# Kernel optimization log

Measured on AMD Instinct MI355X. Metric: run time of the kernel, lower is better.

The kernel has to match this reference:

```python
import jax, jax.numpy as jnp
import numpy as np

B, N, D, R = 4, 2048, 1024, 64
LN_EPS = 1e-5


def setup_inputs() -> dict:
    key = jax.random.key(0)
    k_x, k_m, k_u, k_v = jax.random.split(key, 4)
    x = jax.random.normal(k_x, (B, N, D), dtype=jnp.float32)
    mask = jax.random.uniform(k_m, (B, N, R), dtype=jnp.float32)
    # xavier-style init for low-rank bases U_max, V_max: (d_model, R_max)
    scale = jnp.sqrt(2.0 / (D + R)).astype(jnp.float32)
    U = jax.random.normal(k_u, (D, R), dtype=jnp.float32) * scale
    V = jax.random.normal(k_v, (D, R), dtype=jnp.float32) * scale
    gamma = jnp.ones((D,), dtype=jnp.float32)
    beta = jnp.zeros((D,), dtype=jnp.float32)
    return {"x": x, "mask": mask, "U": U, "V": V, "gamma": gamma, "beta": beta}


def _layernorm(y, gamma, beta):
    mu = jnp.mean(y, axis=-1, keepdims=True)
    var = jnp.mean(jnp.square(y - mu), axis=-1, keepdims=True)
    return (y - mu) * jax.lax.rsqrt(var + LN_EPS) * gamma + beta


def reference(x, mask, U, V, gamma, beta):
    # Q/K: low-rank projections gated by per-token continuous mask
    Q = jnp.einsum('bnd,dr->bnr', x, U) * mask            # (B, N, R)
    K = jnp.einsum('bnd,dr->bnr', x, V) * mask            # (B, N, R)
    # effective rank per query token, clamped at 1
    r_eff = jnp.maximum(jnp.sum(mask, axis=-1, keepdims=True), 1.0)  # (B, N, 1)
    scores = jnp.einsum('bqr,bkr->bqk', Q, K) / jnp.sqrt(r_eff)      # (B, N, N)
    A = jax.nn.softmax(scores, axis=-1)
    delta = jnp.einsum('bqk,bkd->bqd', A, x)              # (B, N, D)
    # backbone is identity: out = LN(x + delta)
    return _layernorm(x + delta, gamma, beta)
```

## Files before the change

kernel.cpp:

```cpp
#include <hip/hip_runtime.h>

#define Bb 4
#define Nn 2048
#define Dd 1024
#define Rr 64
#define LN_EPS 1e-5f

typedef unsigned short u16;
typedef short bf16x8 __attribute__((ext_vector_type(8)));
typedef float f32x4 __attribute__((ext_vector_type(4)));

__device__ __forceinline__ u16 f2bf(float f) {
  unsigned u = __float_as_uint(f);
  u += 0x7FFFu + ((u >> 16) & 1u);
  return (u16)(u >> 16);
}

__device__ __forceinline__ void g2l16(u16* l, const u16* g) {
  __builtin_amdgcn_global_load_lds(
      (const __attribute__((address_space(1))) unsigned int*)g,
      (__attribute__((address_space(3))) unsigned int*)l, 16, 0, 0);
}

__global__ __launch_bounds__(256) void prep_fused(const float* __restrict__ x,
    u16* __restrict__ xt, u16* __restrict__ xb, const float* __restrict__ U,
    const float* __restrict__ V, const float* __restrict__ mask,
    u16* __restrict__ uvt, float* __restrict__ qs) {
  __shared__ float tile[64][65];
  const int bid = blockIdx.x;
  const int t = threadIdx.x;
  if (bid < 2048) {
    const int b = bid >> 9;
    const int d0 = ((bid >> 5) & 15) * 64;
    const int n0 = (bid & 31) * 64;
    const int c = t & 63, r4 = t >> 6;
#pragma unroll
    for (int rr = 0; rr < 16; rr++) {
      int row = rr * 4 + r4;
      tile[row][c] = x[(size_t)(b * Nn + n0 + row) * Dd + d0 + c];
    }
    __syncthreads();
    const int c2 = t & 31, r8 = t >> 5;
#pragma unroll
    for (int rr = 0; rr < 8; rr++) {
      int dd = rr * 8 + r8;
      unsigned lo = f2bf(tile[2 * c2][dd]);
      unsigned hi = f2bf(tile[2 * c2 + 1][dd]);
      *(unsigned*)&xt[(size_t)(b * Dd + d0 + dd) * Nn + n0 + 2 * c2] = lo | (hi << 16);
    }
#pragma unroll
    for (int rr = 0; rr < 8; rr++) {
      int row = rr * 8 + r8;
      unsigned lo = f2bf(tile[row][2 * c2]);
      unsigned hi = f2bf(tile[row][2 * c2 + 1]);
      *(unsigned*)&xb[(size_t)(b * Nn + n0 + row) * Dd + d0 + 2 * c2] = lo | (hi << 16);
    }
  } else if (bid < 2080) {
    const int sub = bid - 2048;
    const int which = sub >> 4;
    const int d0 = (sub & 15) * 64;
    const float* src = which ? V : U;
    const int c = t & 63, r4 = t >> 6;
#pragma unroll
    for (int rr = 0; rr < 16; rr++) {
      int row = rr * 4 + r4;
      tile[row][c] = src[(size_t)(d0 + row) * Rr + c];
    }
    __syncthreads();
#pragma unroll
    for (int rr = 0; rr < 16; rr++) {
      int r = rr * 4 + r4;
      uvt[(size_t)(which * 64 + r) * Dd + d0 + c] = f2bf(tile[c][r]);
    }
  } else {
    const int row = (bid - 2080) * 4 + (t >> 6);
    const int lane = t & 63;
    float v = mask[(size_t)row * Rr + lane];
#pragma unroll
    for (int off = 32; off; off >>= 1) v += __shfl_xor(v, off);
    if (lane == 0) qs[row] = rsqrtf(fmaxf(v, 1.0f));
  }
}

__global__ __launch_bounds__(256) void proj_qk(const u16* __restrict__ xb,
    const float* __restrict__ mask, const u16* __restrict__ uvt,
    u16* __restrict__ Qo, u16* __restrict__ Ko) {
  const int t = threadIdx.x;
  const int w = t >> 6, l = t & 63, quad = l >> 4, l16 = l & 15;
  const int g0 = blockIdx.x * 32;
  f32x4 acc[2][2];
#pragma unroll
  for (int i = 0; i < 2; i++)
#pragma unroll
    for (int j = 0; j < 2; j++) acc[i][j] = (f32x4){0.f, 0.f, 0.f, 0.f};
  for (int k0 = 0; k0 < Dd; k0 += 32) {
    bf16x8 a[2];
#pragma unroll
    for (int mt = 0; mt < 2; mt++)
      a[mt] = *(const bf16x8*)&xb[(size_t)(g0 + mt * 16 + l16) * Dd + k0 + quad * 8];
    bf16x8 bfr[2];
#pragma unroll
    for (int i = 0; i < 2; i++) {
      int col = (w * 2 + i) * 16 + l16;
      bfr[i] = *(const bf16x8*)&uvt[(size_t)col * Dd + k0 + quad * 8];
    }
#pragma unroll
    for (int mt = 0; mt < 2; mt++)
#pragma unroll
      for (int i = 0; i < 2; i++)
        acc[mt][i] = __builtin_amdgcn_mfma_f32_16x16x32_bf16(a[mt], bfr[i], acc[mt][i], 0, 0, 0);
  }
#pragma unroll
  for (int mt = 0; mt < 2; mt++)
#pragma unroll
    for (int i = 0; i < 2; i++) {
      int col = (w * 2 + i) * 16 + l16;
      int r_ = col & 63;
#pragma unroll
      for (int r = 0; r < 4; r++) {
        int row = g0 + mt * 16 + quad * 4 + r;
        float v = acc[mt][i][r] * mask[(size_t)row * Rr + r_];
        u16 bv = f2bf(v);
        if (col < 64) Qo[(size_t)row * Rr + r_] = bv;
        else          Ko[(size_t)row * Rr + r_] = bv;
      }
    }
}

__global__ __launch_bounds__(512, 2) void score_softmax(
    const u16* __restrict__ Qm, const u16* __restrict__ Km,
    const float* __restrict__ qs, u16* __restrict__ Pw,
    float* __restrict__ linv_g) {
  __shared__ float red[32][8];
  __shared__ float mfin[32];
  __shared__ __align__(16) u16 Ps[8][32][264];
  const int t = threadIdx.x;
  const int w = t >> 6, l = t & 63, quad = l >> 4, l16 = l & 15;
  const int id = blockIdx.x;
  const int xcd = id & 7;
  const int b = xcd >> 1;
  const int q0 = (((id >> 3) << 1) | (xcd & 1)) * 32;
  bf16x8 qf[2][2];
#pragma unroll
  for (int mt = 0; mt < 2; mt++)
#pragma unroll
    for (int ks = 0; ks < 2; ks++)
      qf[mt][ks] = *(const bf16x8*)&Qm[(size_t)(b * Nn + q0 + mt * 16 + l16) * Rr + ks * 32 + quad * 8];
  f32x4 acc[2][16];
#pragma unroll
  for (int mt = 0; mt < 2; mt++)
#pragma unroll
    for (int nt = 0; nt < 16; nt++) acc[mt][nt] = (f32x4){0.f, 0.f, 0.f, 0.f};
#pragma unroll
  for (int nt = 0; nt < 16; nt++) {
#pragma unroll
    for (int ks = 0; ks < 2; ks++) {
      bf16x8 kf = *(const bf16x8*)&Km[(size_t)(b * Nn + w * 256 + nt * 16 + l16) * Rr + ks * 32 + quad * 8];
#pragma unroll
      for (int mt = 0; mt < 2; mt++)
        acc[mt][nt] = __builtin_amdgcn_mfma_f32_16x16x32_bf16(qf[mt][ks], kf, acc[mt][nt], 0, 0, 0);
    }
  }
  float sc[2][4];
#pragma unroll
  for (int mt = 0; mt < 2; mt++)
#pragma unroll
    for (int r = 0; r < 4; r++)
      sc[mt][r] = qs[(size_t)b * Nn + q0 + mt * 16 + quad * 4 + r];
#pragma unroll
  for (int mt = 0; mt < 2; mt++)
#pragma unroll
    for (int nt = 0; nt < 16; nt++)
#pragma unroll
      for (int r = 0; r < 4; r++) acc[mt][nt][r] *= sc[mt][r];
  float vmax[2][4];
#pragma unroll
  for (int mt = 0; mt < 2; mt++)
#pragma unroll
    for (int r = 0; r < 4; r++) {
      float m = -1e30f;
#pragma unroll
      for (int nt = 0; nt < 16; nt++) m = fmaxf(m, acc[mt][nt][r]);
#pragma unroll
      for (int off = 1; off < 16; off <<= 1) m = fmaxf(m, __shfl_xor(m, off));
      vmax[mt][r] = m;
    }
  if (l16 == 0) {
#pragma unroll
    for (int mt = 0; mt < 2; mt++)
#pragma unroll
      for (int r = 0; r < 4; r++) red[mt * 16 + quad * 4 + r][w] = vmax[mt][r];
  }
  __syncthreads();
  if (t < 32) {
    float m = -1e30f;
#pragma unroll
    for (int i = 0; i < 8; i++) m = fmaxf(m, red[t][i]);
    mfin[t] = m;
  }
  __syncthreads();
  float rowm[2][4], vsum[2][4];
#pragma unroll
  for (int mt = 0; mt < 2; mt++)
#pragma unroll
    for (int r = 0; r < 4; r++) {
      rowm[mt][r] = mfin[mt * 16 + quad * 4 + r];
      vsum[mt][r] = 0.f;
    }
#pragma unroll
  for (int mt = 0; mt < 2; mt++)
#pragma unroll
    for (int nt = 0; nt < 16; nt++)
#pragma unroll
      for (int r = 0; r < 4; r++) {
        float p = __expf(acc[mt][nt][r] - rowm[mt][r]);
        acc[mt][nt][r] = p;
        vsum[mt][r] += p;
      }
#pragma unroll
  for (int mt = 0; mt < 2; mt++)
#pragma unroll
    for (int r = 0; r < 4; r++) {
#pragma unroll
      for (int off = 1; off < 16; off <<= 1) vsum[mt][r] += __shfl_xor(vsum[mt][r], off);
    }
  __syncthreads();
  if (l16 == 0) {
#pragma unroll
    for (int mt = 0; mt < 2; mt++)
#pragma unroll
      for (int r = 0; r < 4; r++) red[mt * 16 + quad * 4 + r][w] = vsum[mt][r];
  }
  __syncthreads();
  if (t < 32) {
    float s = 0.f;
#pragma unroll
    for (int i = 0; i < 8; i++) s += red[t][i];
    linv_g[(size_t)b * Nn + q0 + t] = 1.f / s;
  }
#pragma unroll
  for (int mt = 0; mt < 2; mt++)
#pragma unroll
    for (int nt = 0; nt < 16; nt++)
#pragma unroll
      for (int r = 0; r < 4; r++)
        Ps[w][mt * 16 + quad * 4 + r][nt * 16 + l16] = f2bf(acc[mt][nt][r]);
  const int rrow = l >> 3, rcol = (l & 7) * 8;
#pragma unroll
  for (int rr = 0; rr < 4; rr++)
#pragma unroll
    for (int cc = 0; cc < 4; cc++) {
      const int row = rr * 8 + rrow;
      const int col = cc * 64 + rcol;
      bf16x8 v = *(const bf16x8*)&Ps[w][row][col];
      *(bf16x8*)&Pw[(size_t)(b * Nn + q0 + row) * Nn + w * 256 + col] = v;
    }
}

__global__ __launch_bounds__(512, 4) void pv_gemm(
    const u16* __restrict__ Pw, const u16* __restrict__ xt,
    const float* __restrict__ x, const float* __restrict__ linv_g,
    float* __restrict__ y) {
  __shared__ u16 As[2][128 * 64];
  __shared__ u16 Bs[2][128 * 64];
  const int t = threadIdx.x;
  const int w = t >> 6, l = t & 63, quad = l >> 4, l16 = l & 15;
  const int id = blockIdx.x;
  const int xcd = id & 7;
  const int b = xcd >> 1;
  const int nh = xcd & 1;
  const int rest = id >> 3;
  const int m0 = (rest & 15) * 128;
  const int n0 = (nh * 4 + (rest >> 4)) * 128;
  const int lrow = l >> 3;
  const int srow = w * 8 + lrow;
  const int skoff = ((l & 7) ^ lrow) * 8;
  const size_t gA = (size_t)(b * Nn + m0 + srow) * Nn + skoff;
  const size_t gB = (size_t)(b * Dd + n0 + srow) * Nn + skoff;
  const int wm = w >> 2, wn = w & 3;
  const int sw = l16 & 7;
  f32x4 acc[4][2];
#pragma unroll
  for (int i = 0; i < 4; i++)
#pragma unroll
    for (int j = 0; j < 2; j++) acc[i][j] = (f32x4){0.f, 0.f, 0.f, 0.f};

#define STAGE(bf, k0)                                              \
  do {                                                             \
    g2l16(&As[bf][(w * 8) * 64],      &Pw[gA + (size_t)(k0)]);     \
    g2l16(&As[bf][(64 + w * 8) * 64], &Pw[gA + 64 * Nn + (size_t)(k0)]); \
    g2l16(&Bs[bf][(w * 8) * 64],      &xt[gB + (size_t)(k0)]);     \
    g2l16(&Bs[bf][(64 + w * 8) * 64], &xt[gB + 64 * Nn + (size_t)(k0)]); \
  } while (0)

  STAGE(0, 0);
  for (int kt = 0; kt < Nn / 64; kt++) {
    const int cur = kt & 1;
    if (kt + 1 < Nn / 64) {
      STAGE(cur ^ 1, (kt + 1) * 64);
      asm volatile("s_waitcnt vmcnt(4)" ::: "memory");
    } else {
      asm volatile("s_waitcnt vmcnt(0)" ::: "memory");
    }
    __builtin_amdgcn_s_barrier();
    asm volatile("" ::: "memory");
#pragma unroll
    for (int ks = 0; ks < 2; ks++) {
      const int slot = ((ks * 4 + quad) ^ sw) * 8;
      bf16x8 af[4], bf_[2];
#pragma unroll
      for (int mt = 0; mt < 4; mt++)
        af[mt] = *(const bf16x8*)&As[cur][(wm * 64 + mt * 16 + l16) * 64 + slot];
#pragma unroll
      for (int nt = 0; nt < 2; nt++)
        bf_[nt] = *(const bf16x8*)&Bs[cur][(wn * 32 + nt * 16 + l16) * 64 + slot];
#pragma unroll
      for (int mt = 0; mt < 4; mt++)
#pragma unroll
        for (int nt = 0; nt < 2; nt++)
          acc[mt][nt] = __builtin_amdgcn_mfma_f32_16x16x32_bf16(af[mt], bf_[nt], acc[mt][nt], 0, 0, 0);
    }
    asm volatile("" ::: "memory");
    __builtin_amdgcn_s_barrier();
  }
#undef STAGE
  float li[4][4];
#pragma unroll
  for (int mt = 0; mt < 4; mt++)
#pragma unroll
    for (int r = 0; r < 4; r++)
      li[mt][r] = linv_g[(size_t)b * Nn + m0 + wm * 64 + mt * 16 + quad * 4 + r];
#pragma unroll
  for (int mt = 0; mt < 4; mt++)
#pragma unroll
    for (int nt = 0; nt < 2; nt++) {
      const int nn = n0 + wn * 32 + nt * 16 + l16;
#pragma unroll
      for (int r = 0; r < 4; r++) {
        const int m = m0 + wm * 64 + mt * 16 + quad * 4 + r;
        const size_t off = ((size_t)(b * Nn + m)) * Dd + nn;
        y[off] = x[off] + li[mt][r] * acc[mt][nt][r];
      }
    }
}

__global__ __launch_bounds__(256) void ln_k(float* __restrict__ y,
    const float* __restrict__ gamma, const float* __restrict__ beta) {
  const int row = blockIdx.x * 4 + (threadIdx.x >> 6);
  const int l = threadIdx.x & 63;
  float* p = y + (size_t)row * Dd;
  float4 v[4];
  float s = 0.f, q = 0.f;
#pragma unroll
  for (int i = 0; i < 4; i++) {
    v[i] = ((const float4*)p)[i * 64 + l];
    s += v[i].x + v[i].y + v[i].z + v[i].w;
    q += v[i].x * v[i].x + v[i].y * v[i].y + v[i].z * v[i].z + v[i].w * v[i].w;
  }
#pragma unroll
  for (int off = 32; off; off >>= 1) {
    s += __shfl_xor(s, off);
    q += __shfl_xor(q, off);
  }
  float mu = s * (1.f / Dd);
  float var = q * (1.f / Dd) - mu * mu;
  float rstd = rsqrtf(var + LN_EPS);
#pragma unroll
  for (int i = 0; i < 4; i++) {
    float4 g = ((const float4*)gamma)[i * 64 + l];
    float4 be = ((const float4*)beta)[i * 64 + l];
    v[i].x = (v[i].x - mu) * rstd * g.x + be.x;
    v[i].y = (v[i].y - mu) * rstd * g.y + be.y;
    v[i].z = (v[i].z - mu) * rstd * g.z + be.z;
    v[i].w = (v[i].w - mu) * rstd * g.w + be.w;
    ((float4*)p)[i * 64 + l] = v[i];
  }
}

extern "C" void kernel_launch(void* const* d_in, const int* in_sizes, int n_in,
                              void* d_out, int out_size, void* d_ws, size_t ws_size,
                              hipStream_t stream) {
  const float* x     = (const float*)d_in[0];
  const float* mask  = (const float*)d_in[1];
  const float* U     = (const float*)d_in[2];
  const float* V     = (const float*)d_in[3];
  const float* gamma = (const float*)d_in[4];
  const float* beta  = (const float*)d_in[5];
  float* out = (float*)d_out;
  char* ws = (char*)d_ws;
  u16*   xt   = (u16*)ws;
  u16*   Qw   = (u16*)(ws + (size_t)(16 << 20));
  u16*   Kw   = (u16*)(ws + (size_t)(17 << 20));
  u16*   uvt  = (u16*)(ws + (size_t)(18 << 20));
  float* qsb  = (float*)(ws + (size_t)(18 << 20) + (256 << 10));
  float* linv = (float*)(ws + (size_t)(18 << 20) + (288 << 10));
  u16*   Pw   = (u16*)(ws + (size_t)(19 << 20));
  u16*   xb   = Pw;

  prep_fused   <<<4128, 256, 0, stream>>>(x, xt, xb, U, V, mask, uvt, qsb);
  proj_qk      <<<(Bb * Nn) / 32, 256, 0, stream>>>(xb, mask, uvt, Qw, Kw);
  score_softmax<<<Bb * (Nn / 32), 512, 0, stream>>>(Qw, Kw, qsb, Pw, linv);
  pv_gemm      <<<Bb * (Nn / 128) * (Dd / 128), 512, 0, stream>>>(Pw, xt, x, linv, out);
  ln_k         <<<Bb * Nn / 4, 256, 0, stream>>>(out, gamma, beta);
}
```

Before: 185.7 us.

## Recompute QK scores inside PV GEMM instead of materializing probability matrix

The score kernel now computes only the row max and inverse sum and no longer writes the bf16 probability matrix P (B×N×N). The PV kernel recomputes QK^T per 64-key tile with MFMA, applies exp with the stored max, scale and 1/sum, stages P through per-wave LDS, and multiplies it by x. This removes a large write and read of P to and from HBM. In exchange, each n-tile block repeats the score computation (D/128 = 8 times per query row), and the per-warp tiling changes from 4x2 to 1x8 MFMA tiles.

```diff
diff --git a/kernel.cpp b/kernel.cpp
--- a/kernel.cpp
+++ b/kernel.cpp
@@ -127,13 +127,12 @@
     }
 }
 
-__global__ __launch_bounds__(512, 2) void score_softmax(
+__global__ __launch_bounds__(512, 2) void score_ml(
     const u16* __restrict__ Qm, const u16* __restrict__ Km,
-    const float* __restrict__ qs, u16* __restrict__ Pw,
+    const float* __restrict__ qs, float* __restrict__ mx_g,
     float* __restrict__ linv_g) {
-  __shared__ float red[32][8];
-  __shared__ float mfin[32];
-  __shared__ __align__(16) u16 Ps[8][32][264];
+  __shared__ __align__(16) float red[32][8];
+  __shared__ __align__(16) float mfin[32];
   const int t = threadIdx.x;
   const int w = t >> 6, l = t & 63, quad = l >> 4, l16 = l & 15;
   const int id = blockIdx.x;
@@ -197,6 +196,7 @@
 #pragma unroll
     for (int i = 0; i < 8; i++) m = fmaxf(m, red[t][i]);
     mfin[t] = m;
+    mx_g[(size_t)b * Nn + q0 + t] = m;
   }
   __syncthreads();
   float rowm[2][4], vsum[2][4];
@@ -212,11 +212,8 @@
 #pragma unroll
     for (int nt = 0; nt < 16; nt++)
 #pragma unroll
-      for (int r = 0; r < 4; r++) {
-        float p = __expf(acc[mt][nt][r] - rowm[mt][r]);
-        acc[mt][nt][r] = p;
-        vsum[mt][r] += p;
-      }
+      for (int r = 0; r < 4; r++)
+        vsum[mt][r] += __expf(acc[mt][nt][r] - rowm[mt][r]);
 #pragma unroll
   for (int mt = 0; mt < 2; mt++)
 #pragma unroll
@@ -238,31 +235,16 @@
     for (int i = 0; i < 8; i++) s += red[t][i];
     linv_g[(size_t)b * Nn + q0 + t] = 1.f / s;
   }
-#pragma unroll
-  for (int mt = 0; mt < 2; mt++)
-#pragma unroll
-    for (int nt = 0; nt < 16; nt++)
-#pragma unroll
-      for (int r = 0; r < 4; r++)
-        Ps[w][mt * 16 + quad * 4 + r][nt * 16 + l16] = f2bf(acc[mt][nt][r]);
-  const int rrow = l >> 3, rcol = (l & 7) * 8;
-#pragma unroll
-  for (int rr = 0; rr < 4; rr++)
-#pragma unroll
-    for (int cc = 0; cc < 4; cc++) {
-      const int row = rr * 8 + rrow;
-      const int col = cc * 64 + rcol;
-      bf16x8 v = *(const bf16x8*)&Ps[w][row][col];
-      *(bf16x8*)&Pw[(size_t)(b * Nn + q0 + row) * Nn + w * 256 + col] = v;
-    }
-}
-
-__global__ __launch_bounds__(512, 4) void pv_gemm(
-    const u16* __restrict__ Pw, const u16* __restrict__ xt,
-    const float* __restrict__ x, const float* __restrict__ linv_g,
-    float* __restrict__ y) {
-  __shared__ u16 As[2][128 * 64];
-  __shared__ u16 Bs[2][128 * 64];
+}
+
+__global__ __launch_bounds__(512, 4) void pv_fused(
+    const u16* __restrict__ Qw, const u16* __restrict__ Kw,
+    const u16* __restrict__ xt, const float* __restrict__ x,
+    const float* __restrict__ qs, const float* __restrict__ mx_g,
+    const float* __restrict__ linv_g, float* __restrict__ y) {
+  __shared__ __align__(16) u16 Ks[2][64 * 64];
+  __shared__ __align__(16) u16 Xs[2][128 * 64];
+  __shared__ __align__(16) u16 Ps[8][16 * 64];
   const int t = threadIdx.x;
   const int w = t >> 6, l = t & 63, quad = l >> 4, l16 = l & 15;
   const int id = blockIdx.x;
@@ -273,75 +255,90 @@
   const int m0 = (rest & 15) * 128;
   const int n0 = (nh * 4 + (rest >> 4)) * 128;
   const int lrow = l >> 3;
-  const int srow = w * 8 + lrow;
+  const int wrow = w * 8 + lrow;
   const int skoff = ((l & 7) ^ lrow) * 8;
-  const size_t gA = (size_t)(b * Nn + m0 + srow) * Nn + skoff;
-  const size_t gB = (size_t)(b * Dd + n0 + srow) * Nn + skoff;
-  const int wm = w >> 2, wn = w & 3;
+  const size_t gK = (size_t)(b * Nn + wrow) * Rr + skoff;
+  const size_t gX = (size_t)(b * Dd + n0 + wrow) * Nn + skoff;
   const int sw = l16 & 7;
-  f32x4 acc[4][2];
-#pragma unroll
-  for (int i = 0; i < 4; i++)
-#pragma unroll
-    for (int j = 0; j < 2; j++) acc[i][j] = (f32x4){0.f, 0.f, 0.f, 0.f};
-
-#define STAGE(bf, k0)                                              \
-  do {                                                             \
-    g2l16(&As[bf][(w * 8) * 64],      &Pw[gA + (size_t)(k0)]);     \
-    g2l16(&As[bf][(64 + w * 8) * 64], &Pw[gA + 64 * Nn + (size_t)(k0)]); \
-    g2l16(&Bs[bf][(w * 8) * 64],      &xt[gB + (size_t)(k0)]);     \
-    g2l16(&Bs[bf][(64 + w * 8) * 64], &xt[gB + 64 * Nn + (size_t)(k0)]); \
+  float scq[4], mxr[4], lir[4];
+#pragma unroll
+  for (int r = 0; r < 4; r++) {
+    const size_t row = (size_t)b * Nn + m0 + w * 16 + quad * 4 + r;
+    scq[r] = qs[row];
+    mxr[r] = mx_g[row];
+    lir[r] = linv_g[row];
+  }
+  bf16x8 qf[2];
+#pragma unroll
+  for (int ks = 0; ks < 2; ks++)
+    qf[ks] = *(const bf16x8*)&Qw[(size_t)(b * Nn + m0 + w * 16 + l16) * Rr + ks * 32 + quad * 8];
+  f32x4 acc[8];
+#pragma unroll
+  for (int i = 0; i < 8; i++) acc[i] = (f32x4){0.f, 0.f, 0.f, 0.f};
+
+#define STG(bf, kk)                                                  \
+  do {                                                               \
+    g2l16(&Ks[bf][(w * 8) * 64],      &Kw[gK + (size_t)(kk) * Rr]);  \
+    g2l16(&Xs[bf][(w * 8) * 64],      &xt[gX + (size_t)(kk)]);       \
+    g2l16(&Xs[bf][(64 + w * 8) * 64], &xt[gX + 64 * Nn + (size_t)(kk)]); \
   } while (0)
 
-  STAGE(0, 0);
+  STG(0, 0);
   for (int kt = 0; kt < Nn / 64; kt++) {
     const int cur = kt & 1;
     if (kt + 1 < Nn / 64) {
-      STAGE(cur ^ 1, (kt + 1) * 64);
-      asm volatile("s_waitcnt vmcnt(4)" ::: "memory");
+      STG(cur ^ 1, (kt + 1) * 64);
+      asm volatile("s_waitcnt vmcnt(3)" ::: "memory");
     } else {
       asm volatile("s_waitcnt vmcnt(0)" ::: "memory");
     }
     __builtin_amdgcn_s_barrier();
     asm volatile("" ::: "memory");
+    f32x4 s[4];
+#pragma unroll
+    for (int nt = 0; nt < 4; nt++) s[nt] = (f32x4){0.f, 0.f, 0.f, 0.f};
 #pragma unroll
     for (int ks = 0; ks < 2; ks++) {
       const int slot = ((ks * 4 + quad) ^ sw) * 8;
-      bf16x8 af[4], bf_[2];
-#pragma unroll
-      for (int mt = 0; mt < 4; mt++)
-        af[mt] = *(const bf16x8*)&As[cur][(wm * 64 + mt * 16 + l16) * 64 + slot];
-#pragma unroll
-      for (int nt = 0; nt < 2; nt++)
-        bf_[nt] = *(const bf16x8*)&Bs[cur][(wn * 32 + nt * 16 + l16) * 64 + slot];
-#pragma unroll
-      for (int mt = 0; mt < 4; mt++)
-#pragma unroll
-        for (int nt = 0; nt < 2; nt++)
-          acc[mt][nt] = __builtin_amdgcn_mfma_f32_16x16x32_bf16(af[mt], bf_[nt], acc[mt][nt], 0, 0, 0);
+#pragma unroll
+      for (int nt = 0; nt < 4; nt++) {
+        bf16x8 kf = *(const bf16x8*)&Ks[cur][(nt * 16 + l16) * 64 + slot];
+        s[nt] = __builtin_amdgcn_mfma_f32_16x16x32_bf16(qf[ks], kf, s[nt], 0, 0, 0);
+      }
+    }
+#pragma unroll
+    for (int nt = 0; nt < 4; nt++)
+#pragma unroll
+      for (int r = 0; r < 4; r++) {
+        float p = __expf(s[nt][r] * scq[r] - mxr[r]) * lir[r];
+        const int key = nt * 16 + l16;
+        const int row = quad * 4 + r;
+        Ps[w][row * 64 + (((key >> 3) ^ (row & 7)) * 8) + (key & 7)] = f2bf(p);
+      }
+#pragma unroll
+    for (int ks = 0; ks < 2; ks++) {
+      const int slot = ((ks * 4 + quad) ^ sw) * 8;
+      bf16x8 af = *(const bf16x8*)&Ps[w][l16 * 64 + slot];
+#pragma unroll
+      for (int nt = 0; nt < 8; nt++) {
+        bf16x8 bfx = *(const bf16x8*)&Xs[cur][(nt * 16 + l16) * 64 + slot];
+        acc[nt] = __builtin_amdgcn_mfma_f32_16x16x32_bf16(af, bfx, acc[nt], 0, 0, 0);
+      }
     }
     asm volatile("" ::: "memory");
     __builtin_amdgcn_s_barrier();
   }
-#undef STAGE
-  float li[4][4];
-#pragma unroll
-  for (int mt = 0; mt < 4; mt++)
-#pragma unroll
-    for (int r = 0; r < 4; r++)
-      li[mt][r] = linv_g[(size_t)b * Nn + m0 + wm * 64 + mt * 16 + quad * 4 + r];
-#pragma unroll
-  for (int mt = 0; mt < 4; mt++)
-#pragma unroll
-    for (int nt = 0; nt < 2; nt++) {
-      const int nn = n0 + wn * 32 + nt * 16 + l16;
-#pragma unroll
-      for (int r = 0; r < 4; r++) {
-        const int m = m0 + wm * 64 + mt * 16 + quad * 4 + r;
-        const size_t off = ((size_t)(b * Nn + m)) * Dd + nn;
-        y[off] = x[off] + li[mt][r] * acc[mt][nt][r];
-      }
-    }
+#undef STG
+#pragma unroll
+  for (int nt = 0; nt < 8; nt++) {
+    const int nn = n0 + nt * 16 + l16;
+#pragma unroll
+    for (int r = 0; r < 4; r++) {
+      const int m = m0 + w * 16 + quad * 4 + r;
+      const size_t off = ((size_t)(b * Nn + m)) * Dd + nn;
+      y[off] = x[off] + acc[nt][r];
+    }
+  }
 }
 
 __global__ __launch_bounds__(256) void ln_k(float* __restrict__ y,
@@ -394,12 +391,13 @@
   u16*   uvt  = (u16*)(ws + (size_t)(18 << 20));
   float* qsb  = (float*)(ws + (size_t)(18 << 20) + (256 << 10));
   float* linv = (float*)(ws + (size_t)(18 << 20) + (288 << 10));
-  u16*   Pw   = (u16*)(ws + (size_t)(19 << 20));
-  u16*   xb   = Pw;
-
-  prep_fused   <<<4128, 256, 0, stream>>>(x, xt, xb, U, V, mask, uvt, qsb);
-  proj_qk      <<<(Bb * Nn) / 32, 256, 0, stream>>>(xb, mask, uvt, Qw, Kw);
-  score_softmax<<<Bb * (Nn / 32), 512, 0, stream>>>(Qw, Kw, qsb, Pw, linv);
-  pv_gemm      <<<Bb * (Nn / 128) * (Dd / 128), 512, 0, stream>>>(Pw, xt, x, linv, out);
-  ln_k         <<<Bb * Nn / 4, 256, 0, stream>>>(out, gamma, beta);
-}
+  float* mxb  = (float*)(ws + (size_t)(18 << 20) + (320 << 10));
+  u16*   xb   = (u16*)(ws + (size_t)(19 << 20));
+
+  prep_fused<<<4128, 256, 0, stream>>>(x, xt, xb, U, V, mask, uvt, qsb);
+  proj_qk   <<<(Bb * Nn) / 32, 256, 0, stream>>>(xb, mask, uvt, Qw, Kw);
+  score_ml  <<<Bb * (Nn / 32), 512, 0, stream>>>(Qw, Kw, qsb, mxb, linv);
+  pv_fused  <<<Bb * (Nn / 128) * (Dd / 128), 512, 0, stream>>>(
+      Qw, Kw, xt, x, qsb, mxb, linv, out);
+  ln_k      <<<Bb * Nn / 4, 256, 0, stream>>>(out, gamma, beta);
+}
```

Measured after the change: 209.9 us. +13.1%, slower.
